# Performance work log

Measured on AMD Instinct MI355X. Metric: run time of the kernel, lower is better.

Reference implementation:

```python
import jax, jax.numpy as jnp
from jax import lax
import numpy as np

T = 49        # number of timesteps (hard-coded in source)
UNITS = 256
QN = 9        # n_basis of the Fourier expansion
DIM = 256     # input feature dim
BATCH = 2048
SQRT2 = float(np.sqrt(2.0))


def fourier_basis(q, t):
    """skfda Fourier basis on domain (0,1): [1, sqrt2*sin(2pi t), sqrt2*cos(2pi t), ...].
    t: (T,) -> (T, q). Assumes q odd (constant + (q-1)/2 sin/cos pairs)."""
    cols = [jnp.ones_like(t)]
    for i in range(1, (q - 1) // 2 + 1):
        w = 2.0 * np.pi * i
        cols.append(SQRT2 * jnp.sin(w * t))
        cols.append(SQRT2 * jnp.cos(w * t))
    return jnp.stack(cols, axis=-1)


def setup_inputs() -> dict:
    key = jax.random.key(0)
    ks = jax.random.split(key, 6)
    cat_dim = DIM + UNITS
    return {
        "x": jax.random.normal(ks[0], (BATCH, T, DIM), dtype=jnp.float32),
        "Wf": jax.random.normal(ks[1], (cat_dim, UNITS), dtype=jnp.float32) * 0.05,
        "Wi": jax.random.normal(ks[2], (cat_dim, UNITS), dtype=jnp.float32) * 0.05,
        "Wc": jax.random.normal(ks[3], (cat_dim, UNITS), dtype=jnp.float32) * 0.05,
        "Wo": jax.random.normal(ks[4], (cat_dim, UNITS), dtype=jnp.float32) * 0.05,
        "Q": jax.random.normal(ks[5], (UNITS, QN * UNITS), dtype=jnp.float32) * 0.05,
    }


def reference(x, Wf, Wi, Wc, Wo, Q):
    # Per-step Fourier basis values Bt (T, q).  block_diag(Bt,...,Bt).T against Q
    # is equivalent to contracting Q.reshape(units, units, q) with Bt.
    tgrid = jnp.linspace(0.0, 1.0, T)
    B = fourier_basis(QN, tgrid)                              # (T, q)
    Qr = Q.reshape(UNITS, UNITS, QN)
    U = jnp.einsum('ijq,tq->tij', Qr, B)                      # (T, units, units)

    def step(c, inp):
        xt, Ut = inp                                          # (B, D), (units, units)
        cat = jnp.concatenate([c, xt], axis=-1)               # Ht := states[0] == c
        f = jax.nn.sigmoid(cat @ Wf)
        i = jax.nn.sigmoid(cat @ Wi)
        g = jax.nn.sigmoid(cat @ Wc)                          # sigmoid, as in source
        c_new = i * g + f * c                                 # Ct := states[0] == c
        o = jnp.tanh(cat @ Wo)                                # tanh, as in source
        s = o * jnp.tanh(c_new)
        h = jnp.tanh(s @ Ut)                                  # time-varying projection
        return c_new, h

    c0 = jnp.zeros((x.shape[0], UNITS), dtype=x.dtype)
    _, hs = lax.scan(step, c0, (jnp.swapaxes(x, 0, 1), U))    # hs: (T, B, units)
    return jnp.swapaxes(hs, 0, 1)                             # (B, T, units)
```

## Files before the change

### kernel.cpp

```cpp
#include <hip/hip_runtime.h>


typedef unsigned short u16;
typedef unsigned int u32;
typedef __attribute__((ext_vector_type(8))) short bf16x8;
typedef __attribute__((ext_vector_type(4))) float f32x4;

#define T_STEPS 49
#define OUT_ROW 12544

__device__ __forceinline__ u16 f2b(float f) {
  u32 u = __float_as_uint(f);
  u += 0x7fffu + ((u >> 16) & 1u);
  return (u16)(u >> 16);
}
__device__ __forceinline__ float b2f(u16 h) { return __uint_as_float(((u32)h) << 16); }
__device__ __forceinline__ float sigm(float z) { return 1.0f / (1.0f + __expf(-z)); }
__device__ __forceinline__ float tanh_f(float z) {
  float e = __expf(-2.0f * fabsf(z));
  float r = (1.0f - e) / (1.0f + e);
  return __builtin_copysignf(r, z);
}

__global__ void pack_w(const float* __restrict__ Wf, const float* __restrict__ Wi,
                       const float* __restrict__ Wc, const float* __restrict__ Wo,
                       u16* __restrict__ WcP, u16* __restrict__ WxP) {
  int n = blockIdx.x, k = threadIdx.x;
  int g = n >> 8, u = n & 255;
  const float* W = (g == 0) ? Wf : (g == 1) ? Wi : (g == 2) ? Wc : Wo;
  WcP[n * 256 + k] = f2b(W[k * 256 + u]);
  WxP[n * 256 + k] = f2b(W[(256 + k) * 256 + u]);
}

__global__ void pack_u(const float* __restrict__ Q, u16* __restrict__ UP) {
  int bx = blockIdx.x;
  int t = bx >> 8, jp = bx & 255, j = threadIdx.x;
  const float* q = Q + j * 2304 + jp * 9;
  float tv = (float)t / 48.0f;
  float acc = q[0];
  const float SQ2 = 1.41421356237f;
#pragma unroll
  for (int i = 1; i <= 4; ++i) {
    float ang = 6.283185307179586f * (float)i * tv;
    acc += SQ2 * (sinf(ang) * q[2 * i - 1] + cosf(ang) * q[2 * i]);
  }
  UP[t * 65536 + jp * 256 + j] = f2b(acc);
}

__global__ __launch_bounds__(256) void xproj_k(const float* __restrict__ x,
                                               const u16* __restrict__ WxP,
                                               u16* __restrict__ xp,
                                               int t0, int ct) {
  __shared__ u16 aLds[64][264];
  int tid = threadIdx.x;
  int m0 = blockIdx.x * 64;
#pragma unroll
  for (int it = 0; it < 16; ++it) {
    int flat = it * 1024 + tid * 4;
    int r = flat >> 8, k = flat & 255;
    int rg = m0 + r;
    int b = rg / ct;
    int tt = rg - b * ct;
    const float4 v = *(const float4*)&x[(b * T_STEPS + (t0 + tt)) * 256 + k];
    u16 tmp[4] = {f2b(v.x), f2b(v.y), f2b(v.z), f2b(v.w)};
    *(uint2*)&aLds[r][k] = *(uint2*)tmp;
  }
  __syncthreads();
  int w = tid >> 6, l = tid & 63, lane15 = l & 15, quad = l >> 4;
  for (int rtp = 0; rtp < 2; ++rtp) {
    bf16x8 af[2][8];
#pragma unroll
    for (int h = 0; h < 2; ++h)
#pragma unroll
      for (int ks = 0; ks < 8; ++ks)
        af[h][ks] = *(const bf16x8*)&aLds[rtp * 32 + h * 16 + lane15][ks * 32 + quad * 8];
    for (int ctl = 0; ctl < 16; ++ctl) {
      const u16* bp = WxP + (w * 256 + ctl * 16 + lane15) * 256 + quad * 8;
      bf16x8 bf[8];
#pragma unroll
      for (int ks = 0; ks < 8; ++ks) bf[ks] = *(const bf16x8*)(bp + ks * 32);
#pragma unroll
      for (int h = 0; h < 2; ++h) {
        f32x4 acc = {0.f, 0.f, 0.f, 0.f};
#pragma unroll
        for (int ks = 0; ks < 8; ++ks)
          acc = __builtin_amdgcn_mfma_f32_16x16x32_bf16(af[h][ks], bf[ks], acc, 0, 0, 0);
        int col = w * 256 + ctl * 16 + lane15;
        int rloc = rtp * 32 + h * 16 + quad * 4;
#pragma unroll
        for (int i = 0; i < 4; ++i)
          xp[(m0 + rloc + i) * 1024 + col] = f2b(acc[i]);
      }
    }
  }
}

__global__ __launch_bounds__(512) void rec_k(const u16* __restrict__ WcP,
                                             const u16* __restrict__ UP,
                                             const u16* __restrict__ xp,
                                             float* __restrict__ out,
                                             float* __restrict__ cstate,
                                             int tA, int tB, int cc) {
  __shared__ float cF[8][256];
  __shared__ u16 cB[16][264];
  __shared__ u16 sB[16][264];
  __shared__ float Z[8][1024];
  int tid = threadIdx.x;
  int b0 = blockIdx.x * 8;
  for (int i = tid; i < 16 * 264; i += 512) {
    ((u16*)cB)[i] = 0;
    ((u16*)sB)[i] = 0;
  }
  for (int i = tid; i < 2048; i += 512) {
    int r = i >> 8, u = i & 255;
    float c0 = (tA == 0) ? 0.0f : cstate[(b0 + r) * 256 + u];
    cF[r][u] = c0;
    cB[r][u] = f2b(c0);
  }
  __syncthreads();
  int w = tid >> 6, l = tid & 63, lane15 = l & 15, quad = l >> 4;

#pragma unroll 1
  for (int t = tA; t < tB; ++t) {
    u16 xpv[4][4];
#pragma unroll
    for (int p = 0; p < 4; ++p) {
      int idx = tid + p * 512;
      int r = idx >> 8, u = idx & 255;
      const u16* xb = xp + ((b0 + r) * cc + (t - tA)) * 1024 + u;
#pragma unroll
      for (int g = 0; g < 4; ++g) xpv[p][g] = xb[g * 256];
    }
    bf16x8 af[8];
#pragma unroll
    for (int ks = 0; ks < 8; ++ks)
      af[ks] = *(const bf16x8*)&cB[lane15][ks * 32 + quad * 8];
#pragma unroll
    for (int c8 = 0; c8 < 8; ++c8) {
      f32x4 acc = {0.f, 0.f, 0.f, 0.f};
      const u16* bp = WcP + (w * 128 + c8 * 16 + lane15) * 256 + quad * 8;
#pragma unroll
      for (int ks = 0; ks < 8; ++ks)
        acc = __builtin_amdgcn_mfma_f32_16x16x32_bf16(af[ks], *(const bf16x8*)(bp + ks * 32), acc, 0, 0, 0);
      if (quad < 2) {
        int col = w * 128 + c8 * 16 + lane15;
#pragma unroll
        for (int i = 0; i < 4; ++i) Z[quad * 4 + i][col] = acc[i];
      }
    }
    __syncthreads();
#pragma unroll
    for (int p = 0; p < 4; ++p) {
      int idx = tid + p * 512;
      int r = idx >> 8, u = idx & 255;
      float zf = Z[r][u] + b2f(xpv[p][0]);
      float zi = Z[r][256 + u] + b2f(xpv[p][1]);
      float zg = Z[r][512 + u] + b2f(xpv[p][2]);
      float zo = Z[r][768 + u] + b2f(xpv[p][3]);
      float f = sigm(zf), ii = sigm(zi), gg = sigm(zg), o = tanh_f(zo);
      float cn = ii * gg + f * cF[r][u];
      cF[r][u] = cn;
      cB[r][u] = f2b(cn);
      float s = o * tanh_f(cn);
      sB[r][u] = f2b(s);
    }
    __syncthreads();
    bf16x8 sf[8];
#pragma unroll
    for (int ks = 0; ks < 8; ++ks)
      sf[ks] = *(const bf16x8*)&sB[lane15][ks * 32 + quad * 8];
#pragma unroll
    for (int c2 = 0; c2 < 2; ++c2) {
      f32x4 acc = {0.f, 0.f, 0.f, 0.f};
      const u16* up = UP + t * 65536 + (w * 32 + c2 * 16 + lane15) * 256 + quad * 8;
#pragma unroll
      for (int ks = 0; ks < 8; ++ks)
        acc = __builtin_amdgcn_mfma_f32_16x16x32_bf16(sf[ks], *(const bf16x8*)(up + ks * 32), acc, 0, 0, 0);
      if (quad < 2) {
        int col = w * 32 + c2 * 16 + lane15;
#pragma unroll
        for (int i = 0; i < 4; ++i)
          out[(b0 + quad * 4 + i) * OUT_ROW + t * 256 + col] = tanh_f(acc[i]);
      }
    }
  }
  if (tB < T_STEPS) {
    for (int i = tid; i < 2048; i += 512) {
      int r = i >> 8, u = i & 255;
      cstate[(b0 + r) * 256 + u] = cF[r][u];
    }
  }
}

extern "C" void kernel_launch(void* const* d_in, const int* in_sizes, int n_in,
                              void* d_out, int out_size, void* d_ws, size_t ws_size,
                              hipStream_t stream) {
  const float* x = (const float*)d_in[0];
  const float* Wf = (const float*)d_in[1];
  const float* Wi = (const float*)d_in[2];
  const float* Wc = (const float*)d_in[3];
  const float* Wo = (const float*)d_in[4];
  const float* Q = (const float*)d_in[5];
  float* out = (float*)d_out;

  char* p = (char*)d_ws;
  u16* WcP = (u16*)p;           p += (size_t)1024 * 256 * 2;
  u16* WxP = (u16*)p;           p += (size_t)1024 * 256 * 2;
  u16* UP = (u16*)p;            p += (size_t)49 * 256 * 256 * 2;
  float* cstate = (float*)p;    p += (size_t)2048 * 256 * 4;
  u16* xpb = (u16*)p;
  size_t used = (size_t)(p - (char*)d_ws);
  size_t rem = (ws_size > used) ? (ws_size - used) : 0;
  const size_t perT = (size_t)2048 * 1024 * 2;
  int CT = (int)(rem / perT);
  if (CT > 49) CT = 49;
  if (CT < 1) CT = 1;

  pack_w<<<dim3(1024), dim3(256), 0, stream>>>(Wf, Wi, Wc, Wo, WcP, WxP);
  pack_u<<<dim3(49 * 256), dim3(256), 0, stream>>>(Q, UP);

  for (int t0 = 0; t0 < T_STEPS; t0 += CT) {
    int cc = (T_STEPS - t0 < CT) ? (T_STEPS - t0) : CT;
    xproj_k<<<dim3(2048 * cc / 64), dim3(256), 0, stream>>>(x, WxP, xpb, t0, cc);
    rec_k<<<dim3(256), dim3(512), 0, stream>>>(WcP, UP, xpb, out, cstate, t0, t0 + cc, cc);
  }
}
```

Before: 1.217 ms.

## Split recurrence across workgroup groups with LDS-resident weights and global barriers

```diff
diff --git a/kernel.cpp b/kernel.cpp
--- a/kernel.cpp
+++ b/kernel.cpp
@@ -8,6 +8,9 @@
 
 #define T_STEPS 49
 #define OUT_ROW 12544
+#define NWG 256
+#define GRPWG 8
+#define SMEM_BYTES 143360
 
 __device__ __forceinline__ u16 f2b(float f) {
   u32 u = __float_as_uint(f);
@@ -20,6 +23,11 @@
   float e = __expf(-2.0f * fabsf(z));
   float r = (1.0f - e) / (1.0f + e);
   return __builtin_copysignf(r, z);
+}
+
+__global__ void init_bar(int* __restrict__ bar) {
+  int i = blockIdx.x * 512 + threadIdx.x;
+  if (i < 2048) bar[i] = 0;
 }
 
 __global__ void pack_w(const float* __restrict__ Wf, const float* __restrict__ Wi,
@@ -32,163 +40,184 @@
   WxP[n * 256 + k] = f2b(W[(256 + k) * 256 + u]);
 }
 
-__global__ void pack_u(const float* __restrict__ Q, u16* __restrict__ UP) {
-  int bx = blockIdx.x;
-  int t = bx >> 8, jp = bx & 255, j = threadIdx.x;
-  const float* q = Q + j * 2304 + jp * 9;
-  float tv = (float)t / 48.0f;
-  float acc = q[0];
+__global__ void pack_u2(const float* __restrict__ Q, u16* __restrict__ UP) {
+  int jp = blockIdx.x, j = threadIdx.x;
+  float q[9];
+#pragma unroll
+  for (int k = 0; k < 9; ++k) q[k] = Q[j * 2304 + jp * 9 + k];
   const float SQ2 = 1.41421356237f;
-#pragma unroll
-  for (int i = 1; i <= 4; ++i) {
-    float ang = 6.283185307179586f * (float)i * tv;
-    acc += SQ2 * (sinf(ang) * q[2 * i - 1] + cosf(ang) * q[2 * i]);
-  }
-  UP[t * 65536 + jp * 256 + j] = f2b(acc);
-}
-
-__global__ __launch_bounds__(256) void xproj_k(const float* __restrict__ x,
-                                               const u16* __restrict__ WxP,
-                                               u16* __restrict__ xp,
-                                               int t0, int ct) {
-  __shared__ u16 aLds[64][264];
+  for (int t = 0; t < T_STEPS; ++t) {
+    float tv = (float)t / 48.0f;
+    float acc = q[0];
+#pragma unroll
+    for (int i = 1; i <= 4; ++i) {
+      float ang = 6.283185307179586f * (float)i * tv;
+      acc += SQ2 * (sinf(ang) * q[2 * i - 1] + cosf(ang) * q[2 * i]);
+    }
+    UP[t * 65536 + jp * 256 + j] = f2b(acc);
+  }
+}
+
+__global__ __launch_bounds__(256) void xproj2(const float* __restrict__ x,
+                                              const u16* __restrict__ WxP,
+                                              u16* __restrict__ xp) {
+  __shared__ u16 aLds[112][264];
   int tid = threadIdx.x;
-  int m0 = blockIdx.x * 64;
-#pragma unroll
-  for (int it = 0; it < 16; ++it) {
-    int flat = it * 1024 + tid * 4;
-    int r = flat >> 8, k = flat & 255;
-    int rg = m0 + r;
-    int b = rg / ct;
-    int tt = rg - b * ct;
-    const float4 v = *(const float4*)&x[(b * T_STEPS + (t0 + tt)) * 256 + k];
+  int m0 = blockIdx.x * 112;
+#pragma unroll
+  for (int it = 0; it < 28; ++it) {
+    int flat = (it * 256 + tid) * 16;
+    int r = flat >> 10, k = (flat & 1023) >> 2;
+    float4 v = *(const float4*)&x[(size_t)(m0 + r) * 256 + k];
     u16 tmp[4] = {f2b(v.x), f2b(v.y), f2b(v.z), f2b(v.w)};
     *(uint2*)&aLds[r][k] = *(uint2*)tmp;
   }
   __syncthreads();
-  int w = tid >> 6, l = tid & 63, lane15 = l & 15, quad = l >> 4;
-  for (int rtp = 0; rtp < 2; ++rtp) {
-    bf16x8 af[2][8];
-#pragma unroll
-    for (int h = 0; h < 2; ++h)
-#pragma unroll
-      for (int ks = 0; ks < 8; ++ks)
-        af[h][ks] = *(const bf16x8*)&aLds[rtp * 32 + h * 16 + lane15][ks * 32 + quad * 8];
-    for (int ctl = 0; ctl < 16; ++ctl) {
-      const u16* bp = WxP + (w * 256 + ctl * 16 + lane15) * 256 + quad * 8;
-      bf16x8 bf[8];
-#pragma unroll
-      for (int ks = 0; ks < 8; ++ks) bf[ks] = *(const bf16x8*)(bp + ks * 32);
-#pragma unroll
-      for (int h = 0; h < 2; ++h) {
+  int w = tid >> 6, l = tid & 63, l15 = l & 15, quad = l >> 4;
+  for (int ct = 0; ct < 16; ++ct) {
+    int col = w * 256 + ct * 16 + l15;
+    bf16x8 bf[8];
+    const u16* bp = WxP + (size_t)col * 256 + quad * 8;
+#pragma unroll
+    for (int ks = 0; ks < 8; ++ks) bf[ks] = *(const bf16x8*)(bp + ks * 32);
+#pragma unroll
+    for (int rt = 0; rt < 7; ++rt) {
+      f32x4 acc = {0.f, 0.f, 0.f, 0.f};
+#pragma unroll
+      for (int ks = 0; ks < 8; ++ks) {
+        bf16x8 a = *(const bf16x8*)&aLds[rt * 16 + l15][ks * 32 + quad * 8];
+        acc = __builtin_amdgcn_mfma_f32_16x16x32_bf16(a, bf[ks], acc, 0, 0, 0);
+      }
+#pragma unroll
+      for (int ii = 0; ii < 4; ++ii)
+        xp[(size_t)(m0 + rt * 16 + quad * 4 + ii) * 1024 + col] = f2b(acc[ii]);
+    }
+  }
+}
+
+__device__ __forceinline__ void gbar(int* slot) {
+  __syncthreads();
+  if (threadIdx.x == 0) {
+    __hip_atomic_fetch_add(slot, 1, __ATOMIC_ACQ_REL, __HIP_MEMORY_SCOPE_AGENT);
+    while (__hip_atomic_load(slot, __ATOMIC_ACQUIRE, __HIP_MEMORY_SCOPE_AGENT) < GRPWG)
+      __builtin_amdgcn_s_sleep(2);
+  }
+  __syncthreads();
+}
+
+__global__ __launch_bounds__(512) void rec2(const u16* __restrict__ WcP,
+                                            const u16* __restrict__ UP,
+                                            const u16* __restrict__ xp,
+                                            float* __restrict__ out,
+                                            u16* __restrict__ cBg,
+                                            u16* __restrict__ sBg,
+                                            int* __restrict__ bar) {
+  extern __shared__ char smem[];
+  u16(*wLds)[264] = (u16(*)[264])smem;
+  u16(*aStage)[264] = (u16(*)[264])(smem + 67584);
+  float(*Z)[132] = (float(*)[132])(smem + 101376);
+  float(*cF)[32] = (float(*)[32])(smem + 135168);
+
+  int tid = threadIdx.x;
+  int bid = blockIdx.x;
+  int i = bid >> 3, j = bid & 7;
+  int b0 = i * 64, u0 = j * 32;
+
+  for (int c = tid; c < 128 * 32; c += 512) {
+    int col = c >> 5, koff = (c & 31) * 8;
+    int g = col >> 5, uu = col & 31;
+    *(uint4*)&wLds[col][koff] = *(const uint4*)&WcP[(size_t)(g * 256 + u0 + uu) * 256 + koff];
+  }
+#pragma unroll
+  for (int p = 0; p < 4; ++p) {
+    int item = tid + p * 512;
+    cF[item >> 5][item & 31] = 0.0f;
+  }
+  __syncthreads();
+
+  int w = tid >> 6, l = tid & 63, l15 = l & 15, quad = l >> 4;
+  bf16x8 bfr[8];
+#pragma unroll
+  for (int ks = 0; ks < 8; ++ks)
+    bfr[ks] = *(const bf16x8*)&wLds[w * 16 + l15][ks * 32 + quad * 8];
+
+  int prt = w >> 1, pct = w & 1;
+
+#pragma unroll 1
+  for (int t = 0; t < T_STEPS; ++t) {
+    int rd = t & 1, wr = (t + 1) & 1;
+    float xv[4][4];
+#pragma unroll
+    for (int p = 0; p < 4; ++p) {
+      int item = tid + p * 512, r = item >> 5, uu = item & 31;
+      const u16* xb = xp + ((size_t)(b0 + r) * 49 + t) * 1024 + u0 + uu;
+#pragma unroll
+      for (int g = 0; g < 4; ++g) xv[p][g] = b2f(xb[g * 256]);
+    }
+    if (t > 0) {
+#pragma unroll
+      for (int it = 0; it < 4; ++it) {
+        int flat = (it * 512 + tid) * 16;
+        int r = flat >> 9, off = (flat & 511) >> 1;
+        *(uint4*)&aStage[r][off] =
+            *(const uint4*)&cBg[(size_t)rd * 524288 + (size_t)(b0 + r) * 256 + off];
+      }
+      __syncthreads();
+#pragma unroll
+      for (int rt = 0; rt < 4; ++rt) {
         f32x4 acc = {0.f, 0.f, 0.f, 0.f};
 #pragma unroll
-        for (int ks = 0; ks < 8; ++ks)
-          acc = __builtin_amdgcn_mfma_f32_16x16x32_bf16(af[h][ks], bf[ks], acc, 0, 0, 0);
-        int col = w * 256 + ctl * 16 + lane15;
-        int rloc = rtp * 32 + h * 16 + quad * 4;
-#pragma unroll
-        for (int i = 0; i < 4; ++i)
-          xp[(m0 + rloc + i) * 1024 + col] = f2b(acc[i]);
-      }
-    }
-  }
-}
-
-__global__ __launch_bounds__(512) void rec_k(const u16* __restrict__ WcP,
-                                             const u16* __restrict__ UP,
-                                             const u16* __restrict__ xp,
-                                             float* __restrict__ out,
-                                             float* __restrict__ cstate,
-                                             int tA, int tB, int cc) {
-  __shared__ float cF[8][256];
-  __shared__ u16 cB[16][264];
-  __shared__ u16 sB[16][264];
-  __shared__ float Z[8][1024];
-  int tid = threadIdx.x;
-  int b0 = blockIdx.x * 8;
-  for (int i = tid; i < 16 * 264; i += 512) {
-    ((u16*)cB)[i] = 0;
-    ((u16*)sB)[i] = 0;
-  }
-  for (int i = tid; i < 2048; i += 512) {
-    int r = i >> 8, u = i & 255;
-    float c0 = (tA == 0) ? 0.0f : cstate[(b0 + r) * 256 + u];
-    cF[r][u] = c0;
-    cB[r][u] = f2b(c0);
-  }
-  __syncthreads();
-  int w = tid >> 6, l = tid & 63, lane15 = l & 15, quad = l >> 4;
-
-#pragma unroll 1
-  for (int t = tA; t < tB; ++t) {
-    u16 xpv[4][4];
+        for (int ks = 0; ks < 8; ++ks) {
+          bf16x8 a = *(const bf16x8*)&aStage[rt * 16 + l15][ks * 32 + quad * 8];
+          acc = __builtin_amdgcn_mfma_f32_16x16x32_bf16(a, bfr[ks], acc, 0, 0, 0);
+        }
+#pragma unroll
+        for (int ii = 0; ii < 4; ++ii) Z[rt * 16 + quad * 4 + ii][w * 16 + l15] = acc[ii];
+      }
+      __syncthreads();
+    }
 #pragma unroll
     for (int p = 0; p < 4; ++p) {
-      int idx = tid + p * 512;
-      int r = idx >> 8, u = idx & 255;
-      const u16* xb = xp + ((b0 + r) * cc + (t - tA)) * 1024 + u;
-#pragma unroll
-      for (int g = 0; g < 4; ++g) xpv[p][g] = xb[g * 256];
-    }
-    bf16x8 af[8];
-#pragma unroll
-    for (int ks = 0; ks < 8; ++ks)
-      af[ks] = *(const bf16x8*)&cB[lane15][ks * 32 + quad * 8];
-#pragma unroll
-    for (int c8 = 0; c8 < 8; ++c8) {
+      int item = tid + p * 512, r = item >> 5, uu = item & 31;
+      float zf = xv[p][0], zi = xv[p][1], zg = xv[p][2], zo = xv[p][3];
+      if (t > 0) {
+        zf += Z[r][uu];
+        zi += Z[r][32 + uu];
+        zg += Z[r][64 + uu];
+        zo += Z[r][96 + uu];
+      }
+      float f = sigm(zf), ig = sigm(zi), gg = sigm(zg), o = tanh_f(zo);
+      float cn = ig * gg + f * cF[r][uu];
+      cF[r][uu] = cn;
+      float s = o * tanh_f(cn);
+      size_t gi = (size_t)wr * 524288 + (size_t)(b0 + r) * 256 + u0 + uu;
+      cBg[gi] = f2b(cn);
+      sBg[gi] = f2b(s);
+    }
+    gbar(bar + i * 64 + t);
+#pragma unroll
+    for (int it = 0; it < 4; ++it) {
+      int flat = (it * 512 + tid) * 16;
+      int r = flat >> 9, off = (flat & 511) >> 1;
+      *(uint4*)&aStage[r][off] =
+          *(const uint4*)&sBg[(size_t)wr * 524288 + (size_t)(b0 + r) * 256 + off];
+    }
+    __syncthreads();
+    {
       f32x4 acc = {0.f, 0.f, 0.f, 0.f};
-      const u16* bp = WcP + (w * 128 + c8 * 16 + lane15) * 256 + quad * 8;
-#pragma unroll
-      for (int ks = 0; ks < 8; ++ks)
-        acc = __builtin_amdgcn_mfma_f32_16x16x32_bf16(af[ks], *(const bf16x8*)(bp + ks * 32), acc, 0, 0, 0);
-      if (quad < 2) {
-        int col = w * 128 + c8 * 16 + lane15;
-#pragma unroll
-        for (int i = 0; i < 4; ++i) Z[quad * 4 + i][col] = acc[i];
-      }
+      const u16* up = UP + t * 65536 + (size_t)(u0 + pct * 16 + l15) * 256 + quad * 8;
+#pragma unroll
+      for (int ks = 0; ks < 8; ++ks) {
+        bf16x8 a = *(const bf16x8*)&aStage[prt * 16 + l15][ks * 32 + quad * 8];
+        bf16x8 b = *(const bf16x8*)(up + ks * 32);
+        acc = __builtin_amdgcn_mfma_f32_16x16x32_bf16(a, b, acc, 0, 0, 0);
+      }
+#pragma unroll
+      for (int ii = 0; ii < 4; ++ii)
+        out[(size_t)(b0 + prt * 16 + quad * 4 + ii) * OUT_ROW + t * 256 + u0 + pct * 16 + l15] =
+            tanh_f(acc[ii]);
     }
     __syncthreads();
-#pragma unroll
-    for (int p = 0; p < 4; ++p) {
-      int idx = tid + p * 512;
-      int r = idx >> 8, u = idx & 255;
-      float zf = Z[r][u] + b2f(xpv[p][0]);
-      float zi = Z[r][256 + u] + b2f(xpv[p][1]);
-      float zg = Z[r][512 + u] + b2f(xpv[p][2]);
-      float zo = Z[r][768 + u] + b2f(xpv[p][3]);
-      float f = sigm(zf), ii = sigm(zi), gg = sigm(zg), o = tanh_f(zo);
-      float cn = ii * gg + f * cF[r][u];
-      cF[r][u] = cn;
-      cB[r][u] = f2b(cn);
-      float s = o * tanh_f(cn);
-      sB[r][u] = f2b(s);
-    }
-    __syncthreads();
-    bf16x8 sf[8];
-#pragma unroll
-    for (int ks = 0; ks < 8; ++ks)
-      sf[ks] = *(const bf16x8*)&sB[lane15][ks * 32 + quad * 8];
-#pragma unroll
-    for (int c2 = 0; c2 < 2; ++c2) {
-      f32x4 acc = {0.f, 0.f, 0.f, 0.f};
-      const u16* up = UP + t * 65536 + (w * 32 + c2 * 16 + lane15) * 256 + quad * 8;
-#pragma unroll
-      for (int ks = 0; ks < 8; ++ks)
-        acc = __builtin_amdgcn_mfma_f32_16x16x32_bf16(sf[ks], *(const bf16x8*)(up + ks * 32), acc, 0, 0, 0);
-      if (quad < 2) {
-        int col = w * 32 + c2 * 16 + lane15;
-#pragma unroll
-        for (int i = 0; i < 4; ++i)
-          out[(b0 + quad * 4 + i) * OUT_ROW + t * 256 + col] = tanh_f(acc[i]);
-      }
-    }
-  }
-  if (tB < T_STEPS) {
-    for (int i = tid; i < 2048; i += 512) {
-      int r = i >> 8, u = i & 255;
-      cstate[(b0 + r) * 256 + u] = cF[r][u];
-    }
   }
 }
 
@@ -204,24 +233,24 @@
   float* out = (float*)d_out;
 
   char* p = (char*)d_ws;
-  u16* WcP = (u16*)p;           p += (size_t)1024 * 256 * 2;
-  u16* WxP = (u16*)p;           p += (size_t)1024 * 256 * 2;
-  u16* UP = (u16*)p;            p += (size_t)49 * 256 * 256 * 2;
-  float* cstate = (float*)p;    p += (size_t)2048 * 256 * 4;
-  u16* xpb = (u16*)p;
-  size_t used = (size_t)(p - (char*)d_ws);
-  size_t rem = (ws_size > used) ? (ws_size - used) : 0;
-  const size_t perT = (size_t)2048 * 1024 * 2;
-  int CT = (int)(rem / perT);
-  if (CT > 49) CT = 49;
-  if (CT < 1) CT = 1;
-
+  u16* WcP = (u16*)p;  p += (size_t)1024 * 256 * 2;
+  u16* WxP = (u16*)p;  p += (size_t)1024 * 256 * 2;
+  u16* UP = (u16*)p;   p += (size_t)49 * 65536 * 2;
+  u16* cBg = (u16*)p;  p += (size_t)2 * 524288 * 2;
+  u16* sBg = (u16*)p;  p += (size_t)2 * 524288 * 2;
+  int* bar = (int*)p;  p += 8192;
+  u16* xp = (u16*)p;
+
+  hipFuncSetAttribute((const void*)rec2, hipFuncAttributeMaxDynamicSharedMemorySize,
+                      SMEM_BYTES);
+
+  init_bar<<<dim3(4), dim3(512), 0, stream>>>(bar);
   pack_w<<<dim3(1024), dim3(256), 0, stream>>>(Wf, Wi, Wc, Wo, WcP, WxP);
-  pack_u<<<dim3(49 * 256), dim3(256), 0, stream>>>(Q, UP);
-
-  for (int t0 = 0; t0 < T_STEPS; t0 += CT) {
-    int cc = (T_STEPS - t0 < CT) ? (T_STEPS - t0) : CT;
-    xproj_k<<<dim3(2048 * cc / 64), dim3(256), 0, stream>>>(x, WxP, xpb, t0, cc);
-    rec_k<<<dim3(256), dim3(512), 0, stream>>>(WcP, UP, xpb, out, cstate, t0, t0 + cc, cc);
-  }
-}
+  pack_u2<<<dim3(256), dim3(256), 0, stream>>>(Q, UP);
+  xproj2<<<dim3(896), dim3(256), 0, stream>>>(x, WxP, xp);
+
+  void* args[] = {(void*)&WcP, (void*)&UP, (void*)&xp, (void*)&out,
+                  (void*)&cBg, (void*)&sBg, (void*)&bar};
+  hipLaunchCooperativeKernel((const void*)rec2, dim3(NWG), dim3(512), args,
+                             SMEM_BYTES, stream);
+}
```

Measured after the change: 1.422 ms. +16.8%, slower.

## Stage recurrent weights in LDS, fix time chunking, coalesce outputs

Applied to the files above, without the earlier changes.

```diff
diff --git a/kernel.cpp b/kernel.cpp
--- a/kernel.cpp
+++ b/kernel.cpp
@@ -7,7 +7,19 @@
 typedef __attribute__((ext_vector_type(4))) float f32x4;
 
 #define T_STEPS 49
+#define CT 7
 #define OUT_ROW 12544
+#define STASH_COLS 160
+
+#define OFF_CB   84480
+#define OFF_SB   92928
+#define OFF_CF   101376
+#define OFF_Z    109568
+#define OFF_H    142336
+#define REC_SMEM 150528
+
+#define OFF_OST  16896
+#define XP_SMEM  82944
 
 __device__ __forceinline__ u16 f2b(float f) {
   u32 u = __float_as_uint(f);
@@ -32,162 +44,194 @@
   WxP[n * 256 + k] = f2b(W[(256 + k) * 256 + u]);
 }
 
-__global__ void pack_u(const float* __restrict__ Q, u16* __restrict__ UP) {
-  int bx = blockIdx.x;
-  int t = bx >> 8, jp = bx & 255, j = threadIdx.x;
-  const float* q = Q + j * 2304 + jp * 9;
-  float tv = (float)t / 48.0f;
-  float acc = q[0];
+__global__ void pack_u2(const float* __restrict__ Q, u16* __restrict__ UP) {
+  int jp = blockIdx.x, j = threadIdx.x;
+  float q[9];
+#pragma unroll
+  for (int k = 0; k < 9; ++k) q[k] = Q[j * 2304 + jp * 9 + k];
   const float SQ2 = 1.41421356237f;
-#pragma unroll
-  for (int i = 1; i <= 4; ++i) {
-    float ang = 6.283185307179586f * (float)i * tv;
-    acc += SQ2 * (sinf(ang) * q[2 * i - 1] + cosf(ang) * q[2 * i]);
-  }
-  UP[t * 65536 + jp * 256 + j] = f2b(acc);
-}
-
-__global__ __launch_bounds__(256) void xproj_k(const float* __restrict__ x,
-                                               const u16* __restrict__ WxP,
-                                               u16* __restrict__ xp,
-                                               int t0, int ct) {
-  __shared__ u16 aLds[64][264];
+  for (int t = 0; t < T_STEPS; ++t) {
+    float tv = (float)t / 48.0f;
+    float acc = q[0];
+#pragma unroll
+    for (int i = 1; i <= 4; ++i) {
+      float ang = 6.283185307179586f * (float)i * tv;
+      acc += SQ2 * (sinf(ang) * q[2 * i - 1] + cosf(ang) * q[2 * i]);
+    }
+    UP[t * 65536 + jp * 256 + j] = f2b(acc);
+  }
+}
+
+__global__ __launch_bounds__(512) void xproj3(const float* __restrict__ x,
+                                              const u16* __restrict__ WxP,
+                                              u16* __restrict__ xp, int t0) {
+  extern __shared__ char smem[];
+  u16(*aLds)[264] = (u16(*)[264])smem;
+  u16(*oSt)[1032] = (u16(*)[1032])(smem + OFF_OST);
   int tid = threadIdx.x;
-  int m0 = blockIdx.x * 64;
-#pragma unroll
-  for (int it = 0; it < 16; ++it) {
-    int flat = it * 1024 + tid * 4;
-    int r = flat >> 8, k = flat & 255;
-    int rg = m0 + r;
-    int b = rg / ct;
-    int tt = rg - b * ct;
-    const float4 v = *(const float4*)&x[(b * T_STEPS + (t0 + tt)) * 256 + k];
+  int m0 = blockIdx.x * 32;
+#pragma unroll
+  for (int it = 0; it < 4; ++it) {
+    int fid = it * 512 + tid;
+    int r = fid >> 6, k4 = fid & 63;
+    int g = m0 + r;
+    int b = g / CT, tt = g - b * CT;
+    float4 v = *(const float4*)&x[((size_t)b * T_STEPS + t0 + tt) * 256 + k4 * 4];
     u16 tmp[4] = {f2b(v.x), f2b(v.y), f2b(v.z), f2b(v.w)};
-    *(uint2*)&aLds[r][k] = *(uint2*)tmp;
+    *(uint2*)&aLds[r][k4 * 4] = *(uint2*)tmp;
   }
   __syncthreads();
-  int w = tid >> 6, l = tid & 63, lane15 = l & 15, quad = l >> 4;
-  for (int rtp = 0; rtp < 2; ++rtp) {
-    bf16x8 af[2][8];
-#pragma unroll
-    for (int h = 0; h < 2; ++h)
-#pragma unroll
-      for (int ks = 0; ks < 8; ++ks)
-        af[h][ks] = *(const bf16x8*)&aLds[rtp * 32 + h * 16 + lane15][ks * 32 + quad * 8];
-    for (int ctl = 0; ctl < 16; ++ctl) {
-      const u16* bp = WxP + (w * 256 + ctl * 16 + lane15) * 256 + quad * 8;
-      bf16x8 bf[8];
-#pragma unroll
-      for (int ks = 0; ks < 8; ++ks) bf[ks] = *(const bf16x8*)(bp + ks * 32);
-#pragma unroll
-      for (int h = 0; h < 2; ++h) {
-        f32x4 acc = {0.f, 0.f, 0.f, 0.f};
-#pragma unroll
-        for (int ks = 0; ks < 8; ++ks)
-          acc = __builtin_amdgcn_mfma_f32_16x16x32_bf16(af[h][ks], bf[ks], acc, 0, 0, 0);
-        int col = w * 256 + ctl * 16 + lane15;
-        int rloc = rtp * 32 + h * 16 + quad * 4;
-#pragma unroll
-        for (int i = 0; i < 4; ++i)
-          xp[(m0 + rloc + i) * 1024 + col] = f2b(acc[i]);
-      }
-    }
-  }
-}
-
-__global__ __launch_bounds__(512) void rec_k(const u16* __restrict__ WcP,
-                                             const u16* __restrict__ UP,
-                                             const u16* __restrict__ xp,
-                                             float* __restrict__ out,
-                                             float* __restrict__ cstate,
-                                             int tA, int tB, int cc) {
-  __shared__ float cF[8][256];
-  __shared__ u16 cB[16][264];
-  __shared__ u16 sB[16][264];
-  __shared__ float Z[8][1024];
+  int w = tid >> 6, l = tid & 63, l15 = l & 15, quad = l >> 4;
+#pragma unroll 1
+  for (int c8 = 0; c8 < 8; ++c8) {
+    int col = w * 128 + c8 * 16 + l15;
+    bf16x8 bf[8];
+    const u16* bp = WxP + (size_t)col * 256 + quad * 8;
+#pragma unroll
+    for (int ks = 0; ks < 8; ++ks) bf[ks] = *(const bf16x8*)(bp + ks * 32);
+#pragma unroll
+    for (int rt = 0; rt < 2; ++rt) {
+      f32x4 acc = {0.f, 0.f, 0.f, 0.f};
+#pragma unroll
+      for (int ks = 0; ks < 8; ++ks) {
+        bf16x8 a = *(const bf16x8*)&aLds[rt * 16 + l15][ks * 32 + quad * 8];
+        acc = __builtin_amdgcn_mfma_f32_16x16x32_bf16(a, bf[ks], acc, 0, 0, 0);
+      }
+#pragma unroll
+      for (int i = 0; i < 4; ++i) oSt[rt * 16 + quad * 4 + i][col] = f2b(acc[i]);
+    }
+  }
+  __syncthreads();
+#pragma unroll
+  for (int j = 0; j < 8; ++j) {
+    int e = (j * 512 + tid) * 8;
+    int r = e >> 10, c = e & 1023;
+    *(uint4*)&xp[(size_t)(m0 + r) * 1024 + c] = *(const uint4*)&oSt[r][c];
+  }
+}
+
+__global__ __launch_bounds__(512) void rec3(const u16* __restrict__ WcP,
+                                            const u16* __restrict__ UP,
+                                            const u16* __restrict__ xp,
+                                            float* __restrict__ out,
+                                            float* __restrict__ cstate,
+                                            int tA) {
+  extern __shared__ char smem[];
+  u16(*wLds)[264] = (u16(*)[264])smem;
+  u16(*cB)[264] = (u16(*)[264])(smem + OFF_CB);
+  u16(*sB)[264] = (u16(*)[264])(smem + OFF_SB);
+  float(*cF)[256] = (float(*)[256])(smem + OFF_CF);
+  float(*Z)[1024] = (float(*)[1024])(smem + OFF_Z);
+  float(*hS)[256] = (float(*)[256])(smem + OFF_H);
+
   int tid = threadIdx.x;
   int b0 = blockIdx.x * 8;
+
+  for (int c = tid; c < STASH_COLS * 32; c += 512) {
+    int col = c >> 5, koff = (c & 31) * 8;
+    *(uint4*)&wLds[col][koff] = *(const uint4*)&WcP[(size_t)col * 256 + koff];
+  }
   for (int i = tid; i < 16 * 264; i += 512) {
     ((u16*)cB)[i] = 0;
     ((u16*)sB)[i] = 0;
   }
   for (int i = tid; i < 2048; i += 512) {
     int r = i >> 8, u = i & 255;
-    float c0 = (tA == 0) ? 0.0f : cstate[(b0 + r) * 256 + u];
+    float c0 = (tA == 0) ? 0.0f : cstate[(size_t)(b0 + r) * 256 + u];
     cF[r][u] = c0;
     cB[r][u] = f2b(c0);
   }
   __syncthreads();
-  int w = tid >> 6, l = tid & 63, lane15 = l & 15, quad = l >> 4;
+
+  int w = tid >> 6, l = tid & 63, l15 = l & 15, quad = l >> 4;
 
 #pragma unroll 1
-  for (int t = tA; t < tB; ++t) {
-    u16 xpv[4][4];
+  for (int tt = 0; tt < CT; ++tt) {
+    int t = tA + tt;
+    float xv[4][4];
 #pragma unroll
     for (int p = 0; p < 4; ++p) {
-      int idx = tid + p * 512;
-      int r = idx >> 8, u = idx & 255;
-      const u16* xb = xp + ((b0 + r) * cc + (t - tA)) * 1024 + u;
-#pragma unroll
-      for (int g = 0; g < 4; ++g) xpv[p][g] = xb[g * 256];
-    }
-    bf16x8 af[8];
-#pragma unroll
-    for (int ks = 0; ks < 8; ++ks)
-      af[ks] = *(const bf16x8*)&cB[lane15][ks * 32 + quad * 8];
-#pragma unroll
-    for (int c8 = 0; c8 < 8; ++c8) {
-      f32x4 acc = {0.f, 0.f, 0.f, 0.f};
-      const u16* bp = WcP + (w * 128 + c8 * 16 + lane15) * 256 + quad * 8;
+      int item = tid + p * 512, r = item >> 8, u = item & 255;
+      const u16* xb = xp + ((size_t)(b0 + r) * CT + tt) * 1024 + u;
+#pragma unroll
+      for (int g = 0; g < 4; ++g) xv[p][g] = b2f(xb[g * 256]);
+    }
+    if (t > 0) {
+      bf16x8 af[8];
 #pragma unroll
       for (int ks = 0; ks < 8; ++ks)
-        acc = __builtin_amdgcn_mfma_f32_16x16x32_bf16(af[ks], *(const bf16x8*)(bp + ks * 32), acc, 0, 0, 0);
-      if (quad < 2) {
-        int col = w * 128 + c8 * 16 + lane15;
-#pragma unroll
-        for (int i = 0; i < 4; ++i) Z[quad * 4 + i][col] = acc[i];
-      }
-    }
-    __syncthreads();
+        af[ks] = *(const bf16x8*)&cB[l15][ks * 32 + quad * 8];
+#pragma unroll
+      for (int c8 = 0; c8 < 8; ++c8) {
+        int tb = w * 128 + c8 * 16;
+        f32x4 acc = {0.f, 0.f, 0.f, 0.f};
+        if (tb < STASH_COLS) {
+          const u16* bp = &wLds[tb + l15][quad * 8];
+#pragma unroll
+          for (int ks = 0; ks < 8; ++ks)
+            acc = __builtin_amdgcn_mfma_f32_16x16x32_bf16(
+                af[ks], *(const bf16x8*)(bp + ks * 32), acc, 0, 0, 0);
+        } else {
+          const u16* bp = WcP + (size_t)(tb + l15) * 256 + quad * 8;
+#pragma unroll
+          for (int ks = 0; ks < 8; ++ks)
+            acc = __builtin_amdgcn_mfma_f32_16x16x32_bf16(
+                af[ks], *(const bf16x8*)(bp + ks * 32), acc, 0, 0, 0);
+        }
+        if (quad < 2) {
+          int col = tb + l15;
+#pragma unroll
+          for (int i = 0; i < 4; ++i) Z[quad * 4 + i][col] = acc[i];
+        }
+      }
+      __syncthreads();
+    }
 #pragma unroll
     for (int p = 0; p < 4; ++p) {
-      int idx = tid + p * 512;
-      int r = idx >> 8, u = idx & 255;
-      float zf = Z[r][u] + b2f(xpv[p][0]);
-      float zi = Z[r][256 + u] + b2f(xpv[p][1]);
-      float zg = Z[r][512 + u] + b2f(xpv[p][2]);
-      float zo = Z[r][768 + u] + b2f(xpv[p][3]);
-      float f = sigm(zf), ii = sigm(zi), gg = sigm(zg), o = tanh_f(zo);
-      float cn = ii * gg + f * cF[r][u];
+      int item = tid + p * 512, r = item >> 8, u = item & 255;
+      float zf = xv[p][0], zi = xv[p][1], zg = xv[p][2], zo = xv[p][3];
+      if (t > 0) {
+        zf += Z[r][u];
+        zi += Z[r][256 + u];
+        zg += Z[r][512 + u];
+        zo += Z[r][768 + u];
+      }
+      float f = sigm(zf), ig = sigm(zi), gg = sigm(zg), o = tanh_f(zo);
+      float cn = ig * gg + f * cF[r][u];
       cF[r][u] = cn;
       cB[r][u] = f2b(cn);
-      float s = o * tanh_f(cn);
-      sB[r][u] = f2b(s);
+      sB[r][u] = f2b(o * tanh_f(cn));
     }
     __syncthreads();
     bf16x8 sf[8];
 #pragma unroll
     for (int ks = 0; ks < 8; ++ks)
-      sf[ks] = *(const bf16x8*)&sB[lane15][ks * 32 + quad * 8];
+      sf[ks] = *(const bf16x8*)&sB[l15][ks * 32 + quad * 8];
 #pragma unroll
     for (int c2 = 0; c2 < 2; ++c2) {
       f32x4 acc = {0.f, 0.f, 0.f, 0.f};
-      const u16* up = UP + t * 65536 + (w * 32 + c2 * 16 + lane15) * 256 + quad * 8;
+      const u16* up = UP + (size_t)t * 65536 + (size_t)(w * 32 + c2 * 16 + l15) * 256 + quad * 8;
 #pragma unroll
       for (int ks = 0; ks < 8; ++ks)
-        acc = __builtin_amdgcn_mfma_f32_16x16x32_bf16(sf[ks], *(const bf16x8*)(up + ks * 32), acc, 0, 0, 0);
+        acc = __builtin_amdgcn_mfma_f32_16x16x32_bf16(
+            sf[ks], *(const bf16x8*)(up + ks * 32), acc, 0, 0, 0);
       if (quad < 2) {
-        int col = w * 32 + c2 * 16 + lane15;
-#pragma unroll
-        for (int i = 0; i < 4; ++i)
-          out[(b0 + quad * 4 + i) * OUT_ROW + t * 256 + col] = tanh_f(acc[i]);
-      }
-    }
-  }
-  if (tB < T_STEPS) {
+        int col = w * 32 + c2 * 16 + l15;
+#pragma unroll
+        for (int i = 0; i < 4; ++i) hS[quad * 4 + i][col] = tanh_f(acc[i]);
+      }
+    }
+    __syncthreads();
+    {
+      int r = tid >> 6, c = (tid & 63) * 4;
+      float4 v = *(const float4*)&hS[r][c];
+      *(float4*)&out[(size_t)(b0 + r) * OUT_ROW + (size_t)t * 256 + c] = v;
+    }
+  }
+  if (tA + CT < T_STEPS) {
     for (int i = tid; i < 2048; i += 512) {
       int r = i >> 8, u = i & 255;
-      cstate[(b0 + r) * 256 + u] = cF[r][u];
+      cstate[(size_t)(b0 + r) * 256 + u] = cF[r][u];
     }
   }
 }
@@ -204,24 +248,23 @@
   float* out = (float*)d_out;
 
   char* p = (char*)d_ws;
-  u16* WcP = (u16*)p;           p += (size_t)1024 * 256 * 2;
-  u16* WxP = (u16*)p;           p += (size_t)1024 * 256 * 2;
-  u16* UP = (u16*)p;            p += (size_t)49 * 256 * 256 * 2;
-  float* cstate = (float*)p;    p += (size_t)2048 * 256 * 4;
-  u16* xpb = (u16*)p;
-  size_t used = (size_t)(p - (char*)d_ws);
-  size_t rem = (ws_size > used) ? (ws_size - used) : 0;
-  const size_t perT = (size_t)2048 * 1024 * 2;
-  int CT = (int)(rem / perT);
-  if (CT > 49) CT = 49;
-  if (CT < 1) CT = 1;
+  u16* WcP = (u16*)p;     p += (size_t)1024 * 256 * 2;
+  u16* WxP = (u16*)p;     p += (size_t)1024 * 256 * 2;
+  u16* UP = (u16*)p;      p += (size_t)49 * 65536 * 2;
+  float* cstate = (float*)p; p += (size_t)2048 * 256 * 4;
+  u16* xp = (u16*)p;
+
+  hipFuncSetAttribute((const void*)rec3, hipFuncAttributeMaxDynamicSharedMemorySize,
+                      REC_SMEM);
+  hipFuncSetAttribute((const void*)xproj3, hipFuncAttributeMaxDynamicSharedMemorySize,
+                      XP_SMEM);
 
   pack_w<<<dim3(1024), dim3(256), 0, stream>>>(Wf, Wi, Wc, Wo, WcP, WxP);
-  pack_u<<<dim3(49 * 256), dim3(256), 0, stream>>>(Q, UP);
-
-  for (int t0 = 0; t0 < T_STEPS; t0 += CT) {
-    int cc = (T_STEPS - t0 < CT) ? (T_STEPS - t0) : CT;
-    xproj_k<<<dim3(2048 * cc / 64), dim3(256), 0, stream>>>(x, WxP, xpb, t0, cc);
-    rec_k<<<dim3(256), dim3(512), 0, stream>>>(WcP, UP, xpb, out, cstate, t0, t0 + cc, cc);
-  }
-}
+  pack_u2<<<dim3(256), dim3(256), 0, stream>>>(Q, UP);
+
+  for (int ch = 0; ch < 7; ++ch) {
+    int t0 = ch * CT;
+    xproj3<<<dim3(448), dim3(512), XP_SMEM, stream>>>(x, WxP, xp, t0);
+    rec3<<<dim3(256), dim3(512), REC_SMEM, stream>>>(WcP, UP, xp, out, cstate, t0);
+  }
+}
```

Result: slower. 1.373 ms (+12.8%).
